# Performance work log

Hardware: AMD Instinct MI355X
Metric: run time of the kernel (lower is better)

Reference implementation:

```python
import jax, jax.numpy as jnp
import numpy as np

M, K, CH = 4, 256, 256
D = CH // M  # per-group dim = 64


def _conv(x, w, b, stride=2):
    # x: [N,C,H,W], w: [O,I,kh,kw]
    y = jax.lax.conv_general_dilated(
        x, w, window_strides=(stride, stride), padding='SAME',
        dimension_numbers=('NCHW', 'OIHW', 'NCHW'))
    return y + b[None, :, None, None]


def _encoder(x, w1, b1, w2, b2, w3, b3, w4, b4):
    x = jax.nn.gelu(_conv(x, w1, b1))
    x = jax.nn.gelu(_conv(x, w2, b2))
    x = jax.nn.gelu(_conv(x, w3, b3))
    return _conv(x, w4, b4)


def setup_inputs() -> dict:
    key = jax.random.key(0)
    ks = jax.random.split(key, 12)
    x = jax.random.uniform(ks[0], (16, 3, 256, 256), jnp.float32)

    def w(k, shape, fan_in):
        return jax.random.normal(k, shape, jnp.float32) * (1.0 / np.sqrt(fan_in))

    w1 = w(ks[1], (64, 3, 3, 3), 3 * 9);    b1 = jnp.zeros((64,), jnp.float32)
    w2 = w(ks[2], (128, 64, 3, 3), 64 * 9); b2 = jnp.zeros((128,), jnp.float32)
    w3 = w(ks[3], (256, 128, 3, 3), 128 * 9); b3 = jnp.zeros((256,), jnp.float32)
    w4 = w(ks[4], (CH, 256, 3, 3), 256 * 9); b4 = jnp.zeros((CH,), jnp.float32)
    codebook = w(ks[5], (M, K, D), D)
    wq = w(ks[6], (M, D, D), D)
    wk = w(ks[7], (M, D, D), D)
    return dict(x=x, w1=w1, b1=b1, w2=w2, b2=b2, w3=w3, b3=b3, w4=w4, b4=b4,
                codebook=codebook, wq=wq, wk=wk)


def reference(x, w1, b1, w2, b2, w3, b3, w4, b4, codebook, wq, wk):
    x = (x - 0.5) / 0.5
    n, c, h, w = x.shape  # c == 3 here, so the c==1 expand branch is skipped
    hPad = max(0, 32 - h)
    wPad = max(0, 32 - w)
    if hPad or wPad:
        x = jnp.pad(x, ((0, 0), (0, 0), (0, hPad), (0, wPad)))
    latent = _encoder(x, w1, b1, w2, b2, w3, b3, w4, b4)  # [n, CH, h/16, w/16]
    n2, _, hh, ww = latent.shape
    q = latent.transpose(0, 2, 3, 1).reshape(n2, hh, ww, M, D)
    q = jnp.einsum('nhwmd,mcd->nhwmc', q, wq)            # per-group query proj
    kproj = jnp.einsum('mkd,mcd->mkc', codebook, wk)     # per-group key proj
    scores = jnp.einsum('nhwmd,mkd->nhwmk', q, kproj)    # [n,hh,ww,m,k]
    code = jnp.argmax(scores, axis=-1).astype(jnp.uint8)
    return code, jnp.array([h, w], dtype=jnp.int32)
```

## Files before the change

kernel.cpp:

```cpp
#include <hip/hip_runtime.h>
#include <math.h>


typedef _Float16 half8 __attribute__((ext_vector_type(8)));
typedef float floatx4 __attribute__((ext_vector_type(4)));
typedef unsigned int u32;
typedef unsigned short u16;

__device__ __forceinline__ float gelu_tanh(float x) {
    float x3 = x * x * x;
    float t = 1.5957691216057308f * x + 0.07135481627333636f * x3;
    return x / (1.0f + __expf(-t));
}

__device__ __forceinline__ u32 pack_split(float v) {
    _Float16 h = (_Float16)v;
    _Float16 l = (_Float16)((v - (float)h) * 4096.0f);
    union { _Float16 f; u16 s; } a, b;
    a.f = h; b.f = l;
    return (u32)a.s | ((u32)b.s << 16);
}

template <int Ci, int Co>
__global__ void prep_w(const float* __restrict__ W, _Float16* __restrict__ dH,
                       _Float16* __restrict__ dL) {
    constexpr int KC = Ci / 32, NTg = Co / 16;
    int lin = blockIdx.x * 256 + threadIdx.x;
    if (lin >= 9 * KC * NTg * 64) return;
    int l = lin & 63;
    int q = lin >> 6;
    int nt = q % NTg; q /= NTg;
    int kc = q % KC;
    int tap = q / KC;
    int co = nt * 16 + (l & 15);
    int ci0 = kc * 32 + ((l >> 4) << 3);
#pragma unroll
    for (int j = 0; j < 8; ++j) {
        float v = W[((size_t)co * Ci + ci0 + j) * 9 + tap];
        _Float16 h = (_Float16)v;
        _Float16 lo = (_Float16)((v - (float)h) * 4096.0f);
        dH[(size_t)lin * 8 + j] = h;
        dL[(size_t)lin * 8 + j] = lo;
    }
}

__launch_bounds__(256)
__global__ void conv1_k(const float* __restrict__ x, const float* __restrict__ w,
                        const float* __restrict__ bias, u32* __restrict__ out) {
    __shared__ float win[17 * 260];
    __shared__ float wsh[27 * 64];
    const int t = threadIdx.x;
    const int tx = t & 15, ty = (t >> 4) & 7, cz = t >> 7;
    int bx = blockIdx.x;
    const int cg = bx & 3;
    const int oyt = (bx >> 2) & 15;
    const int n = bx >> 6;
    const int co0 = cg * 16 + cz * 8;
    const int oy = oyt * 8 + ty;
    const int ox0 = tx * 8;
    const int iy0 = oyt * 16;

    for (int e = t; e < 27 * 64; e += 256) {
        int co = e & 63, ct = e >> 6;
        wsh[ct * 64 + co] = w[co * 27 + ct];
    }

    float acc[8][8];
#pragma unroll
    for (int c = 0; c < 8; ++c)
#pragma unroll
        for (int p = 0; p < 8; ++p) acc[c][p] = 0.0f;

    for (int ci = 0; ci < 3; ++ci) {
        __syncthreads();
        for (int e = t; e < 17 * 65; e += 256) {
            int r = e / 65, c4 = (e - r * 65) * 4;
            int iy = iy0 + r;
            float4 v = {0.0f, 0.0f, 0.0f, 0.0f};
            if (c4 < 256 && iy < 256) {
                float4 g = *(const float4*)&x[((size_t)(n * 3 + ci) * 256 + iy) * 256 + c4];
                v.x = 2.0f * g.x - 1.0f; v.y = 2.0f * g.y - 1.0f;
                v.z = 2.0f * g.z - 1.0f; v.w = 2.0f * g.w - 1.0f;
            }
            *(float4*)&win[r * 260 + c4] = v;
        }
        __syncthreads();

#pragma unroll
        for (int ky = 0; ky < 3; ++ky) {
            const float* rowp = &win[(2 * ty + ky) * 260 + 16 * tx];
            float rv[20];
#pragma unroll
            for (int q = 0; q < 5; ++q) {
                float4 v4 = *(const float4*)(rowp + 4 * q);
                rv[4 * q + 0] = v4.x; rv[4 * q + 1] = v4.y;
                rv[4 * q + 2] = v4.z; rv[4 * q + 3] = v4.w;
            }
#pragma unroll
            for (int kx = 0; kx < 3; ++kx) {
                const float* wp = &wsh[(ci * 9 + ky * 3 + kx) * 64 + co0];
                float wv[8];
#pragma unroll
                for (int q = 0; q < 2; ++q) {
                    float4 v4 = *(const float4*)(wp + 4 * q);
                    wv[4 * q + 0] = v4.x; wv[4 * q + 1] = v4.y;
                    wv[4 * q + 2] = v4.z; wv[4 * q + 3] = v4.w;
                }
#pragma unroll
                for (int c = 0; c < 8; ++c)
#pragma unroll
                    for (int p = 0; p < 8; ++p)
                        acc[c][p] += rv[2 * p + kx] * wv[c];
            }
        }
    }

    float bj[8];
#pragma unroll
    for (int c = 0; c < 8; ++c) bj[c] = bias[co0 + c];
#pragma unroll
    for (int p = 0; p < 8; ++p) {
        int ox = ox0 + p;
        size_t base = ((size_t)(n * 128 + oy) * 128 + ox) * 64 + co0;
        uint4 s0, s1;
        s0.x = pack_split(gelu_tanh(acc[0][p] + bj[0]));
        s0.y = pack_split(gelu_tanh(acc[1][p] + bj[1]));
        s0.z = pack_split(gelu_tanh(acc[2][p] + bj[2]));
        s0.w = pack_split(gelu_tanh(acc[3][p] + bj[3]));
        s1.x = pack_split(gelu_tanh(acc[4][p] + bj[4]));
        s1.y = pack_split(gelu_tanh(acc[5][p] + bj[5]));
        s1.z = pack_split(gelu_tanh(acc[6][p] + bj[6]));
        s1.w = pack_split(gelu_tanh(acc[7][p] + bj[7]));
        *(uint4*)&out[base] = s0;
        *(uint4*)&out[base + 4] = s1;
    }
}

template <int Ci, int Co, int Hi, int Wi, int NWAVE, int KSPLIT, bool GELU, bool SPLIT>
__launch_bounds__(NWAVE * 64)
__global__ void conv_mfma(const u32* __restrict__ in, const _Float16* __restrict__ WbH,
                          const _Float16* __restrict__ WbL, const float* __restrict__ bias,
                          void* __restrict__ outp) {
    constexpr int Ho = Hi / 2, Wo = Wi / 2;
    constexpr int KC = Ci / 32, NTg = Co / 16;
    constexpr int OYT = Ho / 4, OXT = Wo / 16, CGT = Co / (16 * NWAVE);
    constexpr int WC = 33, CIBP = 40;
    constexpr int NT = NWAVE * 64;
    constexpr int KCS = KC / KSPLIT;
    __shared__ _Float16 AH[9 * WC * CIBP], AL[9 * WC * CIBP];

    const int t = threadIdx.x, l = t & 63, wid = t >> 6;
    const int wm = wid / (NWAVE / 2), wn = wid % (NWAVE / 2);
    int bx = blockIdx.x;
    const int ks = bx % KSPLIT;  bx /= KSPLIT;
    const int cg = bx % CGT;  bx /= CGT;
    const int oxt = bx % OXT; bx /= OXT;
    const int oyt = bx % OYT; bx /= OYT;
    const int n = bx;
    const int oy0 = oyt * 4, ox0 = oxt * 16, co0 = cg * 16 * NWAVE, nt0 = co0 >> 4;
    const int iy0 = oy0 * 2, ix0 = ox0 * 2;

    floatx4 aM[2][2], aX[2][2];
    floatx4 zz = {0.0f, 0.0f, 0.0f, 0.0f};
#pragma unroll
    for (int a = 0; a < 2; ++a)
#pragma unroll
        for (int b = 0; b < 2; ++b) { aM[a][b] = zz; aX[a][b] = zz; }

    const int bfrag = (wn * 2) * 512 + l * 8;

    for (int kc = ks * KCS; kc < (ks + 1) * KCS; ++kc) {
        __syncthreads();
        for (int e = t; e < 9 * WC * 4; e += NT) {
            int og = e & 3, px = e >> 2;
            int r = px / WC, cx = px - r * WC;
            int iy = iy0 + r, ix = ix0 + cx;
            union { float4 f4[2]; u32 u[8]; } buf;
            if (iy < Hi && ix < Wi) {
                const float4* g = (const float4*)(in + (((size_t)(n * Hi + iy) * Wi + ix) * Ci + kc * 32 + og * 8));
                buf.f4[0] = g[0]; buf.f4[1] = g[1];
            } else {
#pragma unroll
                for (int k2 = 0; k2 < 8; ++k2) buf.u[k2] = 0;
            }
            union { float4 f4; u16 s[8]; } hh, ll;
#pragma unroll
            for (int k2 = 0; k2 < 8; ++k2) {
                hh.s[k2] = (u16)buf.u[k2];
                ll.s[k2] = (u16)(buf.u[k2] >> 16);
            }
            int off = px * CIBP + og * 8;
            *(float4*)&AH[off] = hh.f4;
            *(float4*)&AL[off] = ll.f4;
        }
        __syncthreads();

#pragma unroll
        for (int tap = 0; tap < 9; ++tap) {
            const size_t src = ((size_t)(tap * KC + kc) * NTg + nt0) * 512 + bfrag;
            half8 bh[2], bl[2];
#pragma unroll
            for (int b = 0; b < 2; ++b) {
                bh[b] = *(const half8*)&WbH[src + b * 512];
                bl[b] = *(const half8*)&WbL[src + b * 512];
            }
            const int ky = tap / 3, kx = tap - ky * 3;
#pragma unroll
            for (int a = 0; a < 2; ++a) {
                int mt = wm * 2 + a;
                int off = ((2 * mt + ky) * WC + 2 * (l & 15) + kx) * CIBP + (l >> 4) * 8;
                half8 ah = *(half8*)&AH[off];
                half8 al = *(half8*)&AL[off];
#pragma unroll
                for (int b = 0; b < 2; ++b) {
                    aM[a][b] = __builtin_amdgcn_mfma_f32_16x16x32_f16(ah, bh[b], aM[a][b], 0, 0, 0);
                    aX[a][b] = __builtin_amdgcn_mfma_f32_16x16x32_f16(ah, bl[b], aX[a][b], 0, 0, 0);
                    aX[a][b] = __builtin_amdgcn_mfma_f32_16x16x32_f16(al, bh[b], aX[a][b], 0, 0, 0);
                }
            }
        }
    }

#pragma unroll
    for (int a = 0; a < 2; ++a) {
        int oy = oy0 + wm * 2 + a;
#pragma unroll
        for (int b = 0; b < 2; ++b) {
            int co = co0 + (wn * 2 + b) * 16 + (l & 15);
            float bj = (KSPLIT == 1) ? bias[co] : 0.0f;
#pragma unroll
            for (int r = 0; r < 4; ++r) {
                int ox = ox0 + (l >> 4) * 4 + r;
                float v = aM[a][b][r] + aX[a][b][r] * (1.0f / 4096.0f) + bj;
                size_t oidx = ((size_t)(n * Ho + oy) * Wo + ox) * Co + co;
                if (KSPLIT > 1) {
                    ((float*)outp)[(size_t)ks * (16 * Ho * Wo * Co) + oidx] = v;
                } else {
                    if (GELU) v = gelu_tanh(v);
                    if (SPLIT) ((u32*)outp)[oidx] = pack_split(v);
                    else       ((float*)outp)[oidx] = v;
                }
            }
        }
    }
}

__global__ void reduce4_k(const float* __restrict__ part,
                          const float* __restrict__ bias,
                          float* __restrict__ out) {
    constexpr int PS4 = 16 * 16 * 16 * 256 / 4;
    int gid = blockIdx.x * 256 + threadIdx.x;
    const float4* p = (const float4*)part;
    float4 s = p[gid];
    float4 q1 = p[PS4 + gid];
    float4 q2 = p[2 * PS4 + gid];
    float4 q3 = p[3 * PS4 + gid];
    s.x += q1.x; s.y += q1.y; s.z += q1.z; s.w += q1.w;
    s.x += q2.x; s.y += q2.y; s.z += q2.z; s.w += q2.w;
    s.x += q3.x; s.y += q3.y; s.z += q3.z; s.w += q3.w;
    float4 b = *(const float4*)&bias[(gid * 4) & 255];
    s.x += b.x; s.y += b.y; s.z += b.z; s.w += b.w;
    ((float4*)out)[gid] = s;
}

__global__ void kproj_kernel(const float* __restrict__ cb,
                             const float* __restrict__ wk,
                             float* __restrict__ kp) {
    int m = blockIdx.x >> 8;
    int k = blockIdx.x & 255;
    int c = threadIdx.x;
    const float* cbp = cb + (size_t)(m * 256 + k) * 64;
    const float* wkp = wk + (size_t)(m * 64 + c) * 64;
    float acc = 0.0f;
#pragma unroll 8
    for (int d = 0; d < 64; ++d) acc += cbp[d] * wkp[d];
    kp[(size_t)(m * 256 + k) * 64 + c] = acc;
}

__global__ void m_kernel(const float* __restrict__ wq,
                         const float* __restrict__ kp,
                         float* __restrict__ M) {
    int m = blockIdx.x >> 8;
    int k = blockIdx.x & 255;
    int d = threadIdx.x;
    const float* kpp = &kp[(size_t)(m * 256 + k) * 64];
    const float* wqp = &wq[(size_t)m * 64 * 64 + d];
    float acc = 0.0f;
#pragma unroll 8
    for (int c = 0; c < 64; ++c) acc += wqp[c * 64] * kpp[c];
    M[((size_t)(m * 256 + k)) * 64 + d] = acc;
}

__launch_bounds__(256)
__global__ void head_kernel(const float* __restrict__ latent,
                            const float* __restrict__ M,
                            int* __restrict__ out) {
    __shared__ float rs[256];
    __shared__ int rk[256];
    const int t = threadIdx.x;
    const int px = t & 3, m = (t >> 2) & 3, kq = t >> 4;
    const int pix = blockIdx.x * 4 + px;

    float4 lr[16];
    const float4* lp = (const float4*)&latent[(size_t)pix * 256 + m * 64];
#pragma unroll
    for (int d = 0; d < 16; ++d) lr[d] = lp[d];

    float best = -INFINITY;
    int bestk = 0;
    const float4* Mp = (const float4*)&M[(size_t)(m * 256 + kq * 16) * 64];
#pragma unroll 4
    for (int kk = 0; kk < 16; ++kk) {
        float s0 = 0.0f, s1 = 0.0f, s2 = 0.0f, s3 = 0.0f;
#pragma unroll
        for (int d = 0; d < 16; ++d) {
            float4 mv = Mp[kk * 16 + d];
            s0 += lr[d].x * mv.x; s1 += lr[d].y * mv.y;
            s2 += lr[d].z * mv.z; s3 += lr[d].w * mv.w;
        }
        float s = (s0 + s1) + (s2 + s3);
        if (s > best) { best = s; bestk = kq * 16 + kk; }
    }
    rs[t] = best; rk[t] = bestk;
    __syncthreads();
    if (kq == 0) {
#pragma unroll
        for (int q = 1; q < 16; ++q) {
            float sv = rs[t + 16 * q];
            int kv = rk[t + 16 * q];
            if (sv > best || (sv == best && kv < bestk)) { best = sv; bestk = kv; }
        }
        out[pix * 4 + m] = bestk;
    }
    if (blockIdx.x == 0 && t == 0) { out[16384] = 256; out[16385] = 256; }
}

extern "C" void kernel_launch(void* const* d_in, const int* in_sizes, int n_in,
                              void* d_out, int out_size, void* d_ws, size_t ws_size,
                              hipStream_t stream) {
    const float* x  = (const float*)d_in[0];
    const float* w1 = (const float*)d_in[1];  const float* b1 = (const float*)d_in[2];
    const float* w2 = (const float*)d_in[3];  const float* b2 = (const float*)d_in[4];
    const float* w3 = (const float*)d_in[5];  const float* b3 = (const float*)d_in[6];
    const float* w4 = (const float*)d_in[7];  const float* b4 = (const float*)d_in[8];
    const float* cb = (const float*)d_in[9];
    const float* wq = (const float*)d_in[10];
    const float* wk = (const float*)d_in[11];
    int* out = (int*)d_out;

    char* ws = (char*)d_ws;
    u32*   buf1 = (u32*)ws;
    u32*   buf2 = (u32*)(ws + 67108864);
    u32*   buf3 = (u32*)(ws + 100663296);
    float* buf4 = (float*)(ws + 117440512);
    float* kp   = (float*)(ws + 121634816);
    float* Mbuf = (float*)(ws + 121634816 + 262144);

    _Float16* w2H = (_Float16*)(ws + 100663296);
    _Float16* w2L = w2H + 9 * 2 * 8 * 512;
    _Float16* w3H = (_Float16*)ws;
    _Float16* w3L = w3H + 9 * 4 * 16 * 512;
    _Float16* w4H = w3L + 9 * 4 * 16 * 512;
    _Float16* w4L = w4H + 9 * 8 * 16 * 512;
    float* part4 = (float*)(ws + 67108864);

    prep_w<64, 128><<<36, 256, 0, stream>>>(w2, w2H, w2L);
    conv1_k<<<1024, 256, 0, stream>>>(x, w1, b1, buf1);
    conv_mfma<64, 128, 128, 128, 8, 1, true, true><<<1024, 512, 0, stream>>>(buf1, w2H, w2L, b2, buf2);
    prep_w<128, 256><<<144, 256, 0, stream>>>(w3, w3H, w3L);
    prep_w<256, 256><<<288, 256, 0, stream>>>(w4, w4H, w4L);
    conv_mfma<128, 256, 64, 64, 8, 1, true, true><<<512, 512, 0, stream>>>(buf2, w3H, w3L, b3, buf3);
    kproj_kernel<<<4 * 256, 64, 0, stream>>>(cb, wk, kp);
    m_kernel<<<4 * 256, 64, 0, stream>>>(wq, kp, Mbuf);
    conv_mfma<256, 256, 32, 32, 4, 4, false, false><<<1024, 256, 0, stream>>>(buf3, w4H, w4L, b4, part4);
    reduce4_k<<<1024, 256, 0, stream>>>(part4, b4, buf4);
    head_kernel<<<1024, 256, 0, stream>>>(buf4, Mbuf, out);
}
```

Before: 278.7 us.

## Register-prefetch next input chunk and precompute load offsets in conv_mfma

Global loads for the input tile are now issued for the next K-chunk right after the shared-memory barrier, so they overlap with the MFMA tap loop instead of stalling before each chunk. Per-thread global and LDS offsets are computed once, outside the K loop, which removes the repeated div/mod index math. The cost is extra registers for the staged uint4 data, which may reduce occupancy. The remainder elements are still loaded synchronously.

```diff
diff --git a/kernel.cpp b/kernel.cpp
--- a/kernel.cpp
+++ b/kernel.cpp
@@ -147,6 +147,9 @@
     constexpr int WC = 33, CIBP = 40;
     constexpr int NT = NWAVE * 64;
     constexpr int KCS = KC / KSPLIT;
+    constexpr int NELEM = 9 * WC * 4;
+    constexpr int NFULL = NELEM / NT;
+    constexpr int NREM = NELEM - NFULL * NT;
     __shared__ _Float16 AH[9 * WC * CIBP], AL[9 * WC * CIBP];
 
     const int t = threadIdx.x, l = t & 63, wid = t >> 6;
@@ -169,31 +172,72 @@
 
     const int bfrag = (wn * 2) * 512 + l * 8;
 
-    for (int kc = ks * KCS; kc < (ks + 1) * KCS; ++kc) {
+    int goff[NFULL + 1], loff[NFULL + 1];
+#pragma unroll
+    for (int i = 0; i <= NFULL; ++i) {
+        int e = t + NT * i;
+        int og = e & 3, px = e >> 2;
+        int r = px / WC, cx = px - r * WC;
+        int iy = iy0 + r, ix = ix0 + cx;
+        bool ok = (e < NELEM) && (iy < Hi) && (ix < Wi);
+        goff[i] = ok ? (((n * Hi + iy) * Wi + ix) * Ci + og * 8) : -1;
+        loff[i] = (e < NELEM) ? (px * CIBP + og * 8) : 0;
+    }
+
+    const int kc0 = ks * KCS, kcEnd = kc0 + KCS;
+    uint4 stage[NFULL][2];
+#pragma unroll
+    for (int i = 0; i < NFULL; ++i) {
+        stage[i][0] = uint4{0, 0, 0, 0};
+        stage[i][1] = uint4{0, 0, 0, 0};
+        if (goff[i] >= 0) {
+            const uint4* g = (const uint4*)(in + (size_t)goff[i] + kc0 * 32);
+            stage[i][0] = g[0]; stage[i][1] = g[1];
+        }
+    }
+
+    for (int kc = kc0; kc < kcEnd; ++kc) {
         __syncthreads();
-        for (int e = t; e < 9 * WC * 4; e += NT) {
-            int og = e & 3, px = e >> 2;
-            int r = px / WC, cx = px - r * WC;
-            int iy = iy0 + r, ix = ix0 + cx;
-            union { float4 f4[2]; u32 u[8]; } buf;
-            if (iy < Hi && ix < Wi) {
-                const float4* g = (const float4*)(in + (((size_t)(n * Hi + iy) * Wi + ix) * Ci + kc * 32 + og * 8));
-                buf.f4[0] = g[0]; buf.f4[1] = g[1];
-            } else {
-#pragma unroll
-                for (int k2 = 0; k2 < 8; ++k2) buf.u[k2] = 0;
-            }
+#pragma unroll
+        for (int i = 0; i < NFULL; ++i) {
+            u32 uu[8];
+            *(uint4*)&uu[0] = stage[i][0];
+            *(uint4*)&uu[4] = stage[i][1];
             union { float4 f4; u16 s[8]; } hh, ll;
 #pragma unroll
             for (int k2 = 0; k2 < 8; ++k2) {
-                hh.s[k2] = (u16)buf.u[k2];
-                ll.s[k2] = (u16)(buf.u[k2] >> 16);
-            }
-            int off = px * CIBP + og * 8;
-            *(float4*)&AH[off] = hh.f4;
-            *(float4*)&AL[off] = ll.f4;
+                hh.s[k2] = (u16)uu[k2];
+                ll.s[k2] = (u16)(uu[k2] >> 16);
+            }
+            *(float4*)&AH[loff[i]] = hh.f4;
+            *(float4*)&AL[loff[i]] = ll.f4;
+        }
+        if (NREM && t < NREM) {
+            u32 uu[8] = {0, 0, 0, 0, 0, 0, 0, 0};
+            if (goff[NFULL] >= 0) {
+                const uint4* g = (const uint4*)(in + (size_t)goff[NFULL] + kc * 32);
+                *(uint4*)&uu[0] = g[0]; *(uint4*)&uu[4] = g[1];
+            }
+            union { float4 f4; u16 s[8]; } hh, ll;
+#pragma unroll
+            for (int k2 = 0; k2 < 8; ++k2) {
+                hh.s[k2] = (u16)uu[k2];
+                ll.s[k2] = (u16)(uu[k2] >> 16);
+            }
+            *(float4*)&AH[loff[NFULL]] = hh.f4;
+            *(float4*)&AL[loff[NFULL]] = ll.f4;
         }
         __syncthreads();
+
+        if (kc + 1 < kcEnd) {
+#pragma unroll
+            for (int i = 0; i < NFULL; ++i) {
+                if (goff[i] >= 0) {
+                    const uint4* g = (const uint4*)(in + (size_t)goff[i] + (kc + 1) * 32);
+                    stage[i][0] = g[0]; stage[i][1] = g[1];
+                }
+            }
+        }
 
 #pragma unroll
         for (int tap = 0; tap < 9; ++tap) {
```

Result: slower. 293.3 us (+5.3%).
